# Kernel tuning notes

Measured on AMD Instinct MI355X. Metric: run time of the kernel, lower is better.

The kernel has to match this reference:

```python
import jax, jax.numpy as jnp
import numpy as np

N = 8192   # number of queries
D = 384    # MiniLM-L3 embedding dim
M = 1024   # number of unique docs (segments)


def setup_inputs() -> dict:
    key = jax.random.key(0)
    k1, k2, k3 = jax.random.split(key, 3)
    emb_q = jax.random.normal(k1, (N, D), dtype=jnp.float32)
    label = jax.random.uniform(k2, (N,), dtype=jnp.float32)  # relevance labels, >0 so group sums are nonzero
    doc_ids = jax.random.randint(k3, (N,), 0, M)              # plays the role of unique(emb_k) inverse indices
    return {"emb_q": emb_q, "label": label, "doc_ids": doc_ids}


def reference(emb_q, label, doc_ids):
    # cosine-similarity matrix between queries
    norm_q = emb_q / jnp.linalg.norm(emb_q, axis=1, keepdims=True)   # [N, D]
    sim = norm_q @ norm_q.T                                          # [N_i, N_q]

    # Original double python loop computes, for each doc group j and each row i:
    #   theta[i, q in group j] = sum_{q' in j} label[q'] * sim[i, q'] / sum_{q' in j} label[q']
    # which is a segment-sum over the column axis grouped by doc, then a gather back.
    weighted = sim * label[None, :]                                  # [N_i, N_q]
    num = jax.ops.segment_sum(weighted.T, doc_ids, num_segments=M)   # [M, N_i]
    den = jax.ops.segment_sum(label, doc_ids, num_segments=M)        # [M]
    theta = (num[doc_ids] / den[doc_ids][:, None]).T                 # [N_i, N_q]
    return theta
```

## Files before the change

kernel.cpp:

```cpp
#include <hip/hip_runtime.h>

#define N_Q   8192
#define DIM   384
#define N_DOC 1024

typedef unsigned short ushort_t;
typedef __attribute__((ext_vector_type(8))) short bf16x8;
typedef __attribute__((ext_vector_type(4))) float f32x4;
typedef __attribute__((ext_vector_type(4))) int i32x4;

__device__ __forceinline__ float bf2f(ushort_t u) {
    union { unsigned i; float f; } c; c.i = ((unsigned)u) << 16; return c.f;
}
__device__ __forceinline__ ushort_t f2bf(float f) {
    union { float f; unsigned u; } c; c.f = f;
    unsigned r = c.u + 0x7FFF + ((c.u >> 16) & 1);
    return (ushort_t)(r >> 16);
}
__device__ __forceinline__ void gload_lds16(const void* g, void* l) {
    __builtin_amdgcn_global_load_lds((const __attribute__((address_space(1))) void*)g,
                                     (__attribute__((address_space(3))) void*)l, 16, 0, 0);
}

#define SS_WAVES 8
__global__ __launch_bounds__(512) void k_segnorm(const float* __restrict__ emb,
                                                 const float* __restrict__ label,
                                                 const int*   __restrict__ ids,
                                                 ushort_t* __restrict__ nqb,
                                                 ushort_t* __restrict__ Hb) {
    __shared__ float pacc[SS_WAVES][DIM];
    __shared__ float pden[SS_WAVES];
    int j    = blockIdx.x;
    int lane = threadIdx.x & 63;
    int w    = threadIdx.x >> 6;
    const int span = N_Q / SS_WAVES;
    int q0 = w * span;

    float acc[6] = {0.f, 0.f, 0.f, 0.f, 0.f, 0.f};
    float den = 0.f;

    int idc = ids[q0 + lane];
    for (int base = q0; base < q0 + span; base += 64) {
        int nb = base + 64;
        int idn = (nb < q0 + span) ? ids[nb + lane] : -1;
        unsigned long long mask = __ballot(idc == j);
        while (mask) {
            int b = __builtin_ctzll(mask);
            mask &= mask - 1;
            int q = base + b;
            float lab = label[q];
            const float* row = emb + (size_t)q * DIM;
            float v[6];
            float ss = 0.f;
#pragma unroll
            for (int t = 0; t < 6; ++t) { v[t] = row[lane + 64 * t]; ss += v[t] * v[t]; }
#pragma unroll
            for (int off = 32; off; off >>= 1) ss += __shfl_xor(ss, off);
            float inv = rsqrtf(ss);
            ushort_t* o = nqb + (size_t)q * DIM;
#pragma unroll
            for (int t = 0; t < 6; ++t) {
                float nv = v[t] * inv;
                acc[t] = fmaf(lab, nv, acc[t]);
                o[lane + 64 * t] = f2bf(nv);
            }
            den += lab;
        }
        idc = idn;
    }
#pragma unroll
    for (int t = 0; t < 6; ++t) pacc[w][lane + 64 * t] = acc[t];
    if (lane == 0) pden[w] = den;
    __syncthreads();

    int d = threadIdx.x;
    if (d < DIM) {
        float s = 0.f, dn = 0.f;
#pragma unroll
        for (int ww = 0; ww < SS_WAVES; ++ww) { s += pacc[ww][d]; dn += pden[ww]; }
        float invd = (dn > 0.f) ? (1.f / dn) : 0.f;
        Hb[(size_t)j * DIM + d] = f2bf(s * invd);
    }
}

#define BM 128
#define BN 128
#define BK 64
#define KQ (DIM / BK)

__global__ __launch_bounds__(256) void k_gemm(const ushort_t* __restrict__ A,
                                              const ushort_t* __restrict__ B,
                                              ushort_t* __restrict__ Tb) {
    __shared__ ushort_t As[2][BM * BK];
    __shared__ ushort_t Bs[2][BN * BK];
    int tid  = threadIdx.x;
    int lane = tid & 63, wid = tid >> 6;
    int wr = wid >> 1, wc = wid & 1;
    int row0 = blockIdx.y * BM, col0 = blockIdx.x * BN;
    int fr = lane & 15, kg = lane >> 4;

    auto stage = [&](int kq, int bf) {
#pragma unroll
        for (int r = 0; r < 4; ++r) {
            int flat = r * 256 + tid;
            int row = flat >> 3, gd = flat & 7;
            int gs = gd ^ (row & 7);
            int wbase = (r * 256 + wid * 64) * 8;
            gload_lds16(A + (size_t)(row0 + row) * DIM + kq * BK + gs * 8, &As[bf][wbase]);
            gload_lds16(B + (size_t)(col0 + row) * DIM + kq * BK + gs * 8, &Bs[bf][wbase]);
        }
    };

    f32x4 acc[4][4];
#pragma unroll
    for (int i = 0; i < 4; ++i)
#pragma unroll
        for (int j = 0; j < 4; ++j) acc[i][j] = (f32x4)0.f;

    stage(0, 0);
    __syncthreads();
    int cur = 0;
    for (int kq = 0; kq < KQ; ++kq) {
        if (kq + 1 < KQ) stage(kq + 1, cur ^ 1);

#pragma unroll
        for (int ks = 0; ks < 2; ++ks) {
            bf16x8 a[4], b[4];
#pragma unroll
            for (int mi = 0; mi < 4; ++mi) {
                int m = wr * 64 + mi * 16 + fr;
                a[mi] = *(const bf16x8*)&As[cur][m * 64 + (((ks * 4 + kg) ^ (m & 7)) << 3)];
            }
#pragma unroll
            for (int ni = 0; ni < 4; ++ni) {
                int n = wc * 64 + ni * 16 + fr;
                b[ni] = *(const bf16x8*)&Bs[cur][n * 64 + (((ks * 4 + kg) ^ (n & 7)) << 3)];
            }
#pragma unroll
            for (int mi = 0; mi < 4; ++mi)
#pragma unroll
                for (int ni = 0; ni < 4; ++ni)
                    acc[mi][ni] = __builtin_amdgcn_mfma_f32_16x16x32_bf16(a[mi], b[ni], acc[mi][ni], 0, 0, 0);
        }
        __syncthreads();
        cur ^= 1;
    }

#pragma unroll
    for (int mi = 0; mi < 4; ++mi)
#pragma unroll
        for (int ni = 0; ni < 4; ++ni)
#pragma unroll
            for (int r = 0; r < 4; ++r)
                Tb[(size_t)(row0 + wr * 64 + mi * 16 + kg * 4 + r) * N_DOC
                   + col0 + wc * 64 + ni * 16 + fr] = f2bf(acc[mi][ni][r]);
}

#define EROWS 8
__global__ __launch_bounds__(256) void k_expand(const ushort_t* __restrict__ Tb,
                                                const int*      __restrict__ ids,
                                                float*          __restrict__ out) {
    __shared__ float trow[EROWS * N_DOC];
    int tid = threadIdx.x;
    int i0  = blockIdx.x * EROWS;

    i32x4 idv[N_Q / 4 / 256];
    const i32x4* id4 = (const i32x4*)ids;
#pragma unroll
    for (int it = 0; it < N_Q / 4 / 256; ++it) idv[it] = id4[it * 256 + tid];

    const bf16x8* Tv = (const bf16x8*)(Tb + (size_t)i0 * N_DOC);
#pragma unroll
    for (int c = 0; c < 4; ++c) {
        int chunk = c * 256 + tid;
        bf16x8 v = Tv[chunk];
        f32x4 lo = { bf2f((ushort_t)v[0]), bf2f((ushort_t)v[1]), bf2f((ushort_t)v[2]), bf2f((ushort_t)v[3]) };
        f32x4 hi = { bf2f((ushort_t)v[4]), bf2f((ushort_t)v[5]), bf2f((ushort_t)v[6]), bf2f((ushort_t)v[7]) };
        *(f32x4*)&trow[chunk * 8]     = lo;
        *(f32x4*)&trow[chunk * 8 + 4] = hi;
    }
    __syncthreads();

#pragma unroll
    for (int it = 0; it < N_Q / 4 / 256; ++it) {
        int q4 = it * 256 + tid;
        i32x4 id = idv[it];
#pragma unroll
        for (int r = 0; r < EROWS; ++r) {
            const float* tr = &trow[r * N_DOC];
            f32x4 v = { tr[id.x], tr[id.y], tr[id.z], tr[id.w] };
            __builtin_nontemporal_store(v, (f32x4*)(out + (size_t)(i0 + r) * N_Q) + q4);
        }
    }
}

extern "C" void kernel_launch(void* const* d_in, const int* in_sizes, int n_in,
                              void* d_out, int out_size, void* d_ws, size_t ws_size,
                              hipStream_t stream) {
    const float* emb   = (const float*)d_in[0];
    const float* label = (const float*)d_in[1];
    const int*   ids   = (const int*)d_in[2];
    float* out = (float*)d_out;

    ushort_t* nqb = (ushort_t*)d_ws;
    ushort_t* Hb  = nqb + (size_t)N_Q * DIM;
    ushort_t* Tb  = Hb + (size_t)N_DOC * DIM;

    k_segnorm<<<N_DOC, 512, 0, stream>>>(emb, label, ids, nqb, Hb);
    k_gemm<<<dim3(N_DOC / BN, N_Q / BM), 256, 0, stream>>>(nqb, Hb, Tb);
    k_expand<<<N_Q / EROWS, 256, 0, stream>>>(Tb, ids, out);
}
```

Before: 75.68 us.

## Shrink GEMM tile to 128x64 and drop LDS double buffering

The GEMM now uses 128x64 output tiles, with each wave computing a 32x64 slice, and a single-buffered LDS stage in place of the double-buffered prefetch. This halves accumulator registers and cuts LDS use, so more workgroups can be resident and the grid doubles to 1024 blocks, which covers the CUs better. In exchange, global loads no longer overlap with MFMA work inside a block, and B-tile reuse per block drops.

New measurement: 74.83 us, median of 2. About the same (-1.1%).

```diff
diff --git a/kernel.cpp b/kernel.cpp
--- a/kernel.cpp
+++ b/kernel.cpp
@@ -83,77 +83,70 @@
     }
 }
 
-#define BM 128
-#define BN 128
-#define BK 64
-#define KQ (DIM / BK)
-
 __global__ __launch_bounds__(256) void k_gemm(const ushort_t* __restrict__ A,
                                               const ushort_t* __restrict__ B,
                                               ushort_t* __restrict__ Tb) {
-    __shared__ ushort_t As[2][BM * BK];
-    __shared__ ushort_t Bs[2][BN * BK];
+    __shared__ ushort_t As[128 * 64];
+    __shared__ ushort_t Bs[64 * 64];
     int tid  = threadIdx.x;
-    int lane = tid & 63, wid = tid >> 6;
-    int wr = wid >> 1, wc = wid & 1;
-    int row0 = blockIdx.y * BM, col0 = blockIdx.x * BN;
+    int lane = tid & 63, w = tid >> 6;
+    int row0 = blockIdx.y * 128, col0 = blockIdx.x * 64;
     int fr = lane & 15, kg = lane >> 4;
 
-    auto stage = [&](int kq, int bf) {
+    f32x4 acc[2][4];
+#pragma unroll
+    for (int i = 0; i < 2; ++i)
+#pragma unroll
+        for (int jj = 0; jj < 4; ++jj) acc[i][jj] = (f32x4)0.f;
+
+    for (int kq = 0; kq < 6; ++kq) {
 #pragma unroll
         for (int r = 0; r < 4; ++r) {
             int flat = r * 256 + tid;
-            int row = flat >> 3, gd = flat & 7;
-            int gs = gd ^ (row & 7);
-            int wbase = (r * 256 + wid * 64) * 8;
-            gload_lds16(A + (size_t)(row0 + row) * DIM + kq * BK + gs * 8, &As[bf][wbase]);
-            gload_lds16(B + (size_t)(col0 + row) * DIM + kq * BK + gs * 8, &Bs[bf][wbase]);
-        }
-    };
-
-    f32x4 acc[4][4];
-#pragma unroll
-    for (int i = 0; i < 4; ++i)
-#pragma unroll
-        for (int j = 0; j < 4; ++j) acc[i][j] = (f32x4)0.f;
-
-    stage(0, 0);
-    __syncthreads();
-    int cur = 0;
-    for (int kq = 0; kq < KQ; ++kq) {
-        if (kq + 1 < KQ) stage(kq + 1, cur ^ 1);
+            int row = flat >> 3, gd = flat & 7, gs = gd ^ (row & 7);
+            gload_lds16(A + (size_t)(row0 + row) * DIM + kq * 64 + gs * 8,
+                        &As[(r * 256 + w * 64) * 8]);
+        }
+#pragma unroll
+        for (int r = 0; r < 2; ++r) {
+            int flat = r * 256 + tid;
+            int row = flat >> 3, gd = flat & 7, gs = gd ^ (row & 7);
+            gload_lds16(B + (size_t)(col0 + row) * DIM + kq * 64 + gs * 8,
+                        &Bs[(r * 256 + w * 64) * 8]);
+        }
+        __syncthreads();
 
 #pragma unroll
         for (int ks = 0; ks < 2; ++ks) {
-            bf16x8 a[4], b[4];
-#pragma unroll
-            for (int mi = 0; mi < 4; ++mi) {
-                int m = wr * 64 + mi * 16 + fr;
-                a[mi] = *(const bf16x8*)&As[cur][m * 64 + (((ks * 4 + kg) ^ (m & 7)) << 3)];
+            int kidx = ks * 4 + kg;
+            bf16x8 a[2], b[4];
+#pragma unroll
+            for (int mi = 0; mi < 2; ++mi) {
+                int m = w * 32 + mi * 16 + fr;
+                a[mi] = *(const bf16x8*)&As[(m * 8 + (kidx ^ (m & 7))) * 8];
             }
 #pragma unroll
             for (int ni = 0; ni < 4; ++ni) {
-                int n = wc * 64 + ni * 16 + fr;
-                b[ni] = *(const bf16x8*)&Bs[cur][n * 64 + (((ks * 4 + kg) ^ (n & 7)) << 3)];
+                int n = ni * 16 + fr;
+                b[ni] = *(const bf16x8*)&Bs[(n * 8 + (kidx ^ (n & 7))) * 8];
             }
 #pragma unroll
-            for (int mi = 0; mi < 4; ++mi)
+            for (int mi = 0; mi < 2; ++mi)
 #pragma unroll
                 for (int ni = 0; ni < 4; ++ni)
                     acc[mi][ni] = __builtin_amdgcn_mfma_f32_16x16x32_bf16(a[mi], b[ni], acc[mi][ni], 0, 0, 0);
         }
         __syncthreads();
-        cur ^= 1;
-    }
-
-#pragma unroll
-    for (int mi = 0; mi < 4; ++mi)
+    }
+
+#pragma unroll
+    for (int mi = 0; mi < 2; ++mi)
 #pragma unroll
         for (int ni = 0; ni < 4; ++ni)
 #pragma unroll
-            for (int r = 0; r < 4; ++r)
-                Tb[(size_t)(row0 + wr * 64 + mi * 16 + kg * 4 + r) * N_DOC
-                   + col0 + wc * 64 + ni * 16 + fr] = f2bf(acc[mi][ni][r]);
+            for (int rr = 0; rr < 4; ++rr)
+                Tb[(size_t)(row0 + w * 32 + mi * 16 + kg * 4 + rr) * N_DOC
+                   + col0 + ni * 16 + fr] = f2bf(acc[mi][ni][rr]);
 }
 
 #define EROWS 8
@@ -207,6 +200,6 @@
     ushort_t* Tb  = Hb + (size_t)N_DOC * DIM;
 
     k_segnorm<<<N_DOC, 512, 0, stream>>>(emb, label, ids, nqb, Hb);
-    k_gemm<<<dim3(N_DOC / BN, N_Q / BM), 256, 0, stream>>>(nqb, Hb, Tb);
+    k_gemm<<<dim3(N_DOC / 64, N_Q / 128), 256, 0, stream>>>(nqb, Hb, Tb);
     k_expand<<<N_Q / EROWS, 256, 0, stream>>>(Tb, ids, out);
 }
```
